# Performance work log

Hardware: AMD Instinct MI355X
Metric: run time of the kernel (lower is better)

## Reference

```python
import jax, jax.numpy as jnp
import numpy as np

BLOCK_SIZE = 32
FP6_E2M3_MAX = 7.5

def _build_fp6_e2m3_grid():
    vals = set()
    for bits in range(64):
        s = (bits >> 5) & 1
        e = (bits >> 3) & 3
        m = bits & 7
        v = (m / 8.0) if e == 0 else (1.0 + m / 8.0) * 2.0 ** (e - 1)
        vals.add(-v if s else v)
    return np.array(sorted(vals), dtype=np.float32)

_GRID = jnp.asarray(_build_fp6_e2m3_grid())  # sorted 1-D fp32 grid (46 unique values)

def _nearest_on_grid(x, grid):
    # round-to-nearest on a sorted grid via searchsorted (matches torch reference)
    idx = jnp.clip(jnp.searchsorted(grid, x), 0, grid.shape[0] - 1)
    idx_lo = jnp.maximum(idx - 1, 0)
    v_hi = grid[idx]
    v_lo = grid[idx_lo]
    return jnp.where(jnp.abs(x - v_lo) <= jnp.abs(x - v_hi), v_lo, v_hi)

def _mx_quantize(t, eps=1e-30):
    # t: (rows, K) fp32, K divisible by BLOCK_SIZE
    rows, K = t.shape
    blocks = t.reshape(rows, K // BLOCK_SIZE, BLOCK_SIZE)
    scales = jnp.maximum(jnp.max(jnp.abs(blocks), axis=-1) / FP6_E2M3_MAX, eps)  # (rows, nb)
    q = _nearest_on_grid(blocks / scales[..., None], _GRID)  # fp6-simulated fp32
    return q, scales

def setup_inputs() -> dict:
    key = jax.random.key(0)
    k1, k2, k3 = jax.random.split(key, 3)
    x = jax.random.normal(k1, (8, 8192, 1024), dtype=jnp.float32)
    weight = jax.random.normal(k2, (1024, 1024), dtype=jnp.float32) * 0.02
    bias = jax.random.normal(k3, (1024,), dtype=jnp.float32) * 0.02
    return {"x": x, "weight": weight, "bias": bias}

def reference(x, weight, bias):
    batch_shape = x.shape[:-1]
    in_features = x.shape[-1]
    x2 = x.astype(jnp.float32).reshape(-1, in_features)      # (N, K)
    w2 = weight.astype(jnp.float32)                           # (J, K)
    xq, xs = _mx_quantize(x2)                                 # (N, nb, bs), (N, nb)
    wq, ws = _mx_quantize(w2)                                 # (J, nb, bs), (J, nb)
    # out[n, j] = sum_b xs[n,b] * ws[j,b] * dot(xq[n,b,:], wq[j,b,:])
    # == dequant(x) @ dequant(w).T  (fold fp32 scales into quantized blocks)
    xd = (xq * xs[..., None]).reshape(x2.shape)
    wd = (wq * ws[..., None]).reshape(w2.shape)
    out = xd @ wd.T + bias
    return out.reshape(*batch_shape, -1)
```

## Files before the change

kernel.cpp:

```cpp
#include <hip/hip_runtime.h>
#include <stdint.h>

#define K_DIM 1024
#define N_DIM 1024
#define M_DIM 65536

typedef __bf16 bf16_t;
typedef __bf16 bf16x8 __attribute__((ext_vector_type(8)));
typedef float f32x4 __attribute__((ext_vector_type(4)));

#define GLOAD_LDS16(g, l) __builtin_amdgcn_global_load_lds( \
    (const __attribute__((address_space(1))) void*)(g),     \
    (__attribute__((address_space(3))) void*)(l), 16, 0, 0)

#define VMCNT(n) asm volatile("s_waitcnt vmcnt(%0)" ::"n"(n) : "memory")
#define LGKM(n) asm volatile("s_waitcnt lgkmcnt(%0)" ::"n"(n) : "memory")
#define SCHEDB() __builtin_amdgcn_sched_barrier(0)

__global__ __launch_bounds__(256) void quant_dequant_kernel(
    const float* __restrict__ in, bf16_t* __restrict__ out, long long nvec) {
  long long i = (long long)blockIdx.x * blockDim.x + threadIdx.x;
  long long stride = (long long)gridDim.x * blockDim.x;
  for (; i < nvec; i += stride) {
    long long base = i * 8;
    f32x4 v0 = *reinterpret_cast<const f32x4*>(in + base);
    f32x4 v1 = *reinterpret_cast<const f32x4*>(in + base + 4);
    float mx = 0.0f;
#pragma unroll
    for (int j = 0; j < 4; ++j) {
      mx = fmaxf(mx, fabsf(v0[j]));
      mx = fmaxf(mx, fabsf(v1[j]));
    }
    mx = fmaxf(mx, __shfl_xor(mx, 1));
    mx = fmaxf(mx, __shfl_xor(mx, 2));
    float s = fmaxf(mx / 7.5f, 1e-30f);
    bf16x8 o;
#pragma unroll
    for (int j = 0; j < 8; ++j) {
      float xv = (j < 4) ? v0[j] : v1[j - 4];
      float y = xv / s;
      float m = fabsf(y);
      float h, hinv;
      if (m < 2.0f)      { h = 0.125f; hinv = 8.0f; }
      else if (m < 4.0f) { h = 0.25f;  hinv = 4.0f; }
      else               { h = 0.5f;   hinv = 2.0f; }
      float n = m * hinv;
      float kf = floorf(n);
      float fr = n - kf;
      float up = (fr > 0.5f || (fr == 0.5f && y < 0.0f)) ? 1.0f : 0.0f;
      float q = fminf((kf + up) * h, 7.5f);
      o[j] = (bf16_t)(copysignf(q, y) * s);
    }
    *reinterpret_cast<bf16x8*>(out + base) = o;
  }
}

__global__ __launch_bounds__(512, 2) void mx_gemm(
    const bf16_t* __restrict__ A, const bf16_t* __restrict__ B,
    const float* __restrict__ bias, float* __restrict__ C) {
  __shared__ char lds[131072];

  const int tid = threadIdx.x;
  const int lane = tid & 63;
  const int wid = tid >> 6;
  const int wm = wid >> 2;
  const int wn = wid & 3;

  const int b = blockIdx.x;
  const int xcd = b & 7;
  const int t = b >> 3;
  const int m_tile = xcd * 32 + (t >> 2);
  const int n_tile = t & 3;

  const int R0 = tid >> 2;
  const int c0 = ((tid & 3) ^ ((tid >> 3) & 3)) * 8;
  const bf16_t* aS0 = A + (size_t)(m_tile * 256 + R0) * K_DIM + c0;
  const bf16_t* aS1 = aS0 + (size_t)128 * K_DIM;
  const bf16_t* bS0 = B + (size_t)(n_tile * 256 + R0) * K_DIM + c0;
  const bf16_t* bS1 = bS0 + (size_t)128 * K_DIM;
  const int dstOff = tid * 16;

#define STAGE(u)                                         \
  {                                                      \
    char* sb_ = lds + ((u) & 3) * 32768;                 \
    const int ko_ = (u) * 32;                            \
    GLOAD_LDS16(aS0 + ko_, sb_ + dstOff);                \
    GLOAD_LDS16(aS1 + ko_, sb_ + 8192 + dstOff);         \
    GLOAD_LDS16(bS0 + ko_, sb_ + 16384 + dstOff);        \
    GLOAD_LDS16(bS1 + ko_, sb_ + 24576 + dstOff);        \
  }

  const int ps = (((lane >> 4) ^ ((lane >> 1) & 3)) << 4);
  const int rowb = (lane & 15) * 64 + ps;
  const int aOff = wm * 8192 + rowb;
  const int bOff = 16384 + wn * 4096 + rowb;

  f32x4 acc[8][4];
#pragma unroll
  for (int i = 0; i < 8; ++i)
#pragma unroll
    for (int j = 0; j < 4; ++j) acc[i][j] = (f32x4)(0.0f);

  bf16x8 bfA[4], bfB[4], afA[4], afB[4], af1[4];

#define PH_A(T, BF, AF0, DO_STG)                                          \
  {                                                                       \
    const char* sb_ = lds + ((T) & 3) * 32768;                            \
    _Pragma("unroll") for (int i = 0; i < 4; ++i) af1[i] =                \
        *reinterpret_cast<const bf16x8*>(sb_ + aOff + 4096 + i * 1024);   \
    if (DO_STG) STAGE((T) + 3);                                           \
    LGKM(4);                                                              \
    SCHEDB();                                                             \
    __builtin_amdgcn_s_setprio(1);                                        \
    _Pragma("unroll") for (int i = 0; i < 4; ++i)                         \
        _Pragma("unroll") for (int j = 0; j < 4; ++j) acc[i][j] =         \
            __builtin_amdgcn_mfma_f32_16x16x32_bf16(AF0[i], BF[j],        \
                                                    acc[i][j], 0, 0, 0);  \
    __builtin_amdgcn_s_setprio(0);                                        \
  }

#define PH_B(T, BF, NBF, NAF0, VMN, DO_PRE)                                  \
  {                                                                          \
    VMCNT(VMN);                                                              \
    LGKM(0);                                                                 \
    __builtin_amdgcn_s_barrier();                                            \
    SCHEDB();                                                                \
    if (DO_PRE) {                                                            \
      const char* sn_ = lds + (((T) + 1) & 3) * 32768;                       \
      _Pragma("unroll") for (int j = 0; j < 4; ++j) NBF[j] =                 \
          *reinterpret_cast<const bf16x8*>(sn_ + bOff + j * 1024);           \
      _Pragma("unroll") for (int i = 0; i < 4; ++i) NAF0[i] =                \
          *reinterpret_cast<const bf16x8*>(sn_ + aOff + i * 1024);           \
    }                                                                        \
    __builtin_amdgcn_s_setprio(1);                                           \
    _Pragma("unroll") for (int i = 0; i < 4; ++i)                            \
        _Pragma("unroll") for (int j = 0; j < 4; ++j) acc[4 + i][j] =        \
            __builtin_amdgcn_mfma_f32_16x16x32_bf16(af1[i], BF[j],           \
                                                    acc[4 + i][j], 0, 0, 0); \
    __builtin_amdgcn_s_setprio(0);                                           \
  }

  STAGE(0);
  STAGE(1);
  STAGE(2);
  VMCNT(8);
  __builtin_amdgcn_s_barrier();
  SCHEDB();
#pragma unroll
  for (int j = 0; j < 4; ++j)
    bfA[j] = *reinterpret_cast<const bf16x8*>(lds + bOff + j * 1024);
#pragma unroll
  for (int i = 0; i < 4; ++i)
    afA[i] = *reinterpret_cast<const bf16x8*>(lds + aOff + i * 1024);

  for (int p = 0; p < 14; ++p) {
    const int u = 2 * p;
    PH_A(u, bfA, afA, true);
    PH_B(u, bfA, bfB, afB, 8, true);
    PH_A(u + 1, bfB, afB, true);
    PH_B(u + 1, bfB, bfA, afA, 8, true);
  }
  PH_A(28, bfA, afA, true);
  PH_B(28, bfA, bfB, afB, 8, true);
  PH_A(29, bfB, afB, false);
  PH_B(29, bfB, bfA, afA, 4, true);
  PH_A(30, bfA, afA, false);
  PH_B(30, bfA, bfB, afB, 0, true);
  PH_A(31, bfB, afB, false);
  LGKM(0);
  SCHEDB();
#pragma unroll
  for (int i = 0; i < 4; ++i)
#pragma unroll
    for (int j = 0; j < 4; ++j)
      acc[4 + i][j] = __builtin_amdgcn_mfma_f32_16x16x32_bf16(
          af1[i], bfB[j], acc[4 + i][j], 0, 0, 0);

  const int col0 = n_tile * 256 + wn * 64 + (lane & 15);
  const int row0 = m_tile * 256 + wm * 128 + ((lane >> 4) << 2);
#pragma unroll
  for (int j = 0; j < 4; ++j) {
    float bv = bias[col0 + j * 16];
#pragma unroll
    for (int m = 0; m < 8; ++m) {
#pragma unroll
      for (int r = 0; r < 4; ++r) {
        C[(size_t)(row0 + m * 16 + r) * N_DIM + col0 + j * 16] =
            acc[m][j][r] + bv;
      }
    }
  }
#undef STAGE
#undef PH_A
#undef PH_B
}

extern "C" void kernel_launch(void* const* d_in, const int* in_sizes, int n_in,
                              void* d_out, int out_size, void* d_ws,
                              size_t ws_size, hipStream_t stream) {
  const float* x = (const float*)d_in[0];
  const float* w = (const float*)d_in[1];
  const float* bias = (const float*)d_in[2];
  float* out = (float*)d_out;

  bf16_t* xd = (bf16_t*)d_ws;
  bf16_t* wd = xd + (size_t)M_DIM * K_DIM;

  quant_dequant_kernel<<<4096, 256, 0, stream>>>(x, xd,
                                                 (long long)M_DIM * K_DIM / 8);
  quant_dequant_kernel<<<512, 256, 0, stream>>>(w, wd,
                                                (long long)K_DIM * N_DIM / 8);

  mx_gemm<<<(M_DIM / 256) * (N_DIM / 256), 512, 0, stream>>>(xd, wd, bias,
                                                             out);
}
```

Baseline: 269.8 us.

## Merge quant launches and restructure GEMM pipeline into split A/B staged phases

The two quant-dequant launches become one kernel whose first 512 blocks handle the weight and the rest handle the activation, saving a launch. The GEMM main loop drops register double-buffering of fragments and now loads B and A fragments from LDS at the start of each phase. Global-to-LDS staging is split into A-half and B-half issues, and extra barriers sit around each MFMA phase. This lowers register pressure and simplifies the loop, but adds barriers and exposes LDS read latency before each MFMA group.

New measurement: 275.2 us. About the same (+2.0%).

```diff
diff --git a/kernel.cpp b/kernel.cpp
--- a/kernel.cpp
+++ b/kernel.cpp
@@ -18,10 +18,21 @@
 #define SCHEDB() __builtin_amdgcn_sched_barrier(0)
 
 __global__ __launch_bounds__(256) void quant_dequant_kernel(
-    const float* __restrict__ in, bf16_t* __restrict__ out, long long nvec) {
-  long long i = (long long)blockIdx.x * blockDim.x + threadIdx.x;
-  long long stride = (long long)gridDim.x * blockDim.x;
-  for (; i < nvec; i += stride) {
+    const float* __restrict__ x, bf16_t* __restrict__ xd, long long nx,
+    const float* __restrict__ w, bf16_t* __restrict__ wd, long long nw) {
+  const float* in;
+  bf16_t* out;
+  long long i, stride, n;
+  if (blockIdx.x < 512) {
+    in = w; out = wd; n = nw;
+    i = (long long)blockIdx.x * blockDim.x + threadIdx.x;
+    stride = 512ll * blockDim.x;
+  } else {
+    in = x; out = xd; n = nx;
+    i = (long long)(blockIdx.x - 512) * blockDim.x + threadIdx.x;
+    stride = (long long)(gridDim.x - 512) * blockDim.x;
+  }
+  for (; i < n; i += stride) {
     long long base = i * 8;
     f32x4 v0 = *reinterpret_cast<const f32x4*>(in + base);
     f32x4 v1 = *reinterpret_cast<const f32x4*>(in + base + 4);
@@ -44,9 +55,9 @@
       if (m < 2.0f)      { h = 0.125f; hinv = 8.0f; }
       else if (m < 4.0f) { h = 0.25f;  hinv = 4.0f; }
       else               { h = 0.5f;   hinv = 2.0f; }
-      float n = m * hinv;
-      float kf = floorf(n);
-      float fr = n - kf;
+      float nn = m * hinv;
+      float kf = floorf(nn);
+      float fr = nn - kf;
       float up = (fr > 0.5f || (fr == 0.5f && y < 0.0f)) ? 1.0f : 0.0f;
       float q = fminf((kf + up) * h, 7.5f);
       o[j] = (bf16_t)(copysignf(q, y) * s);
@@ -80,14 +91,19 @@
   const bf16_t* bS1 = bS0 + (size_t)128 * K_DIM;
   const int dstOff = tid * 16;
 
-#define STAGE(u)                                         \
-  {                                                      \
-    char* sb_ = lds + ((u) & 3) * 32768;                 \
-    const int ko_ = (u) * 32;                            \
-    GLOAD_LDS16(aS0 + ko_, sb_ + dstOff);                \
-    GLOAD_LDS16(aS1 + ko_, sb_ + 8192 + dstOff);         \
-    GLOAD_LDS16(bS0 + ko_, sb_ + 16384 + dstOff);        \
-    GLOAD_LDS16(bS1 + ko_, sb_ + 24576 + dstOff);        \
+#define STAGE_A(u)                                  \
+  {                                                 \
+    char* sd_ = lds + ((u) & 3) * 32768;            \
+    const int ko_ = (u) * 32;                       \
+    GLOAD_LDS16(aS0 + ko_, sd_ + dstOff);           \
+    GLOAD_LDS16(aS1 + ko_, sd_ + 8192 + dstOff);    \
+  }
+#define STAGE_B(u)                                  \
+  {                                                 \
+    char* sd_ = lds + ((u) & 3) * 32768;            \
+    const int ko_ = (u) * 32;                       \
+    GLOAD_LDS16(bS0 + ko_, sd_ + 16384 + dstOff);   \
+    GLOAD_LDS16(bS1 + ko_, sd_ + 24576 + dstOff);   \
   }
 
   const int ps = (((lane >> 4) ^ ((lane >> 1) & 3)) << 4);
@@ -101,80 +117,85 @@
 #pragma unroll
     for (int j = 0; j < 4; ++j) acc[i][j] = (f32x4)(0.0f);
 
-  bf16x8 bfA[4], bfB[4], afA[4], afB[4], af1[4];
-
-#define PH_A(T, BF, AF0, DO_STG)                                          \
+  bf16x8 bf[4], afA[4], afB[4];
+
+#define PH_A(T, VMN, DO_STG)                                              \
   {                                                                       \
     const char* sb_ = lds + ((T) & 3) * 32768;                            \
-    _Pragma("unroll") for (int i = 0; i < 4; ++i) af1[i] =                \
-        *reinterpret_cast<const bf16x8*>(sb_ + aOff + 4096 + i * 1024);   \
-    if (DO_STG) STAGE((T) + 3);                                           \
-    LGKM(4);                                                              \
+    _Pragma("unroll") for (int j = 0; j < 4; ++j) bf[j] =                 \
+        *reinterpret_cast<const bf16x8*>(sb_ + bOff + j * 1024);          \
+    _Pragma("unroll") for (int i = 0; i < 4; ++i) afA[i] =                \
+        *reinterpret_cast<const bf16x8*>(sb_ + aOff + i * 1024);          \
+    if (DO_STG) STAGE_A((T) + 3);                                         \
+    VMCNT(VMN);                                                           \
+    __builtin_amdgcn_s_barrier();                                         \
+    LGKM(0);                                                              \
     SCHEDB();                                                             \
     __builtin_amdgcn_s_setprio(1);                                        \
     _Pragma("unroll") for (int i = 0; i < 4; ++i)                         \
         _Pragma("unroll") for (int j = 0; j < 4; ++j) acc[i][j] =         \
-            __builtin_amdgcn_mfma_f32_16x16x32_bf16(AF0[i], BF[j],        \
+            __builtin_amdgcn_mfma_f32_16x16x32_bf16(afA[i], bf[j],        \
                                                     acc[i][j], 0, 0, 0);  \
     __builtin_amdgcn_s_setprio(0);                                        \
-  }
-
-#define PH_B(T, BF, NBF, NAF0, VMN, DO_PRE)                                  \
+    __builtin_amdgcn_s_barrier();                                         \
+  }
+
+#define PH_B(T, VMN, DO_STG)                                                 \
   {                                                                          \
+    const char* sb_ = lds + ((T) & 3) * 32768;                               \
+    _Pragma("unroll") for (int i = 0; i < 4; ++i) afB[i] =                   \
+        *reinterpret_cast<const bf16x8*>(sb_ + aOff + 4096 + i * 1024);      \
+    if (DO_STG) STAGE_B((T) + 3);                                            \
     VMCNT(VMN);                                                              \
+    __builtin_amdgcn_s_barrier();                                            \
     LGKM(0);                                                                 \
-    __builtin_amdgcn_s_barrier();                                            \
     SCHEDB();                                                                \
-    if (DO_PRE) {                                                            \
-      const char* sn_ = lds + (((T) + 1) & 3) * 32768;                       \
-      _Pragma("unroll") for (int j = 0; j < 4; ++j) NBF[j] =                 \
-          *reinterpret_cast<const bf16x8*>(sn_ + bOff + j * 1024);           \
-      _Pragma("unroll") for (int i = 0; i < 4; ++i) NAF0[i] =                \
-          *reinterpret_cast<const bf16x8*>(sn_ + aOff + i * 1024);           \
-    }                                                                        \
     __builtin_amdgcn_s_setprio(1);                                           \
     _Pragma("unroll") for (int i = 0; i < 4; ++i)                            \
         _Pragma("unroll") for (int j = 0; j < 4; ++j) acc[4 + i][j] =        \
-            __builtin_amdgcn_mfma_f32_16x16x32_bf16(af1[i], BF[j],           \
+            __builtin_amdgcn_mfma_f32_16x16x32_bf16(afB[i], bf[j],           \
                                                     acc[4 + i][j], 0, 0, 0); \
     __builtin_amdgcn_s_setprio(0);                                           \
-  }
-
-  STAGE(0);
-  STAGE(1);
-  STAGE(2);
+    __builtin_amdgcn_s_barrier();                                            \
+  }
+
+  STAGE_A(0); STAGE_B(0);
+  STAGE_A(1); STAGE_B(1);
+  STAGE_A(2); STAGE_B(2);
   VMCNT(8);
   __builtin_amdgcn_s_barrier();
-  SCHEDB();
-#pragma unroll
-  for (int j = 0; j < 4; ++j)
-    bfA[j] = *reinterpret_cast<const bf16x8*>(lds + bOff + j * 1024);
-#pragma unroll
-  for (int i = 0; i < 4; ++i)
-    afA[i] = *reinterpret_cast<const bf16x8*>(lds + aOff + i * 1024);
-
-  for (int p = 0; p < 14; ++p) {
-    const int u = 2 * p;
-    PH_A(u, bfA, afA, true);
-    PH_B(u, bfA, bfB, afB, 8, true);
-    PH_A(u + 1, bfB, afB, true);
-    PH_B(u + 1, bfB, bfA, afA, 8, true);
-  }
-  PH_A(28, bfA, afA, true);
-  PH_B(28, bfA, bfB, afB, 8, true);
-  PH_A(29, bfB, afB, false);
-  PH_B(29, bfB, bfA, afA, 4, true);
-  PH_A(30, bfA, afA, false);
-  PH_B(30, bfA, bfB, afB, 0, true);
-  PH_A(31, bfB, afB, false);
-  LGKM(0);
-  SCHEDB();
-#pragma unroll
-  for (int i = 0; i < 4; ++i)
+
+  for (int kt = 0; kt < 29; ++kt) {
+    PH_A(kt, 8, true);
+    PH_B(kt, 8, true);
+  }
+  PH_A(29, 8, false);
+  PH_B(29, 4, false);
+  PH_A(30, 4, false);
+  PH_B(30, 0, false);
+  {
+    const char* sb_ = lds + (31 & 3) * 32768;
 #pragma unroll
     for (int j = 0; j < 4; ++j)
-      acc[4 + i][j] = __builtin_amdgcn_mfma_f32_16x16x32_bf16(
-          af1[i], bfB[j], acc[4 + i][j], 0, 0, 0);
+      bf[j] = *reinterpret_cast<const bf16x8*>(sb_ + bOff + j * 1024);
+#pragma unroll
+    for (int i = 0; i < 4; ++i)
+      afA[i] = *reinterpret_cast<const bf16x8*>(sb_ + aOff + i * 1024);
+#pragma unroll
+    for (int i = 0; i < 4; ++i)
+      afB[i] = *reinterpret_cast<const bf16x8*>(sb_ + aOff + 4096 + i * 1024);
+    LGKM(0);
+    SCHEDB();
+#pragma unroll
+    for (int i = 0; i < 4; ++i)
+#pragma unroll
+      for (int j = 0; j < 4; ++j) {
+        acc[i][j] = __builtin_amdgcn_mfma_f32_16x16x32_bf16(afA[i], bf[j],
+                                                            acc[i][j], 0, 0, 0);
+        acc[4 + i][j] = __builtin_amdgcn_mfma_f32_16x16x32_bf16(
+            afB[i], bf[j], acc[4 + i][j], 0, 0, 0);
+      }
+  }
 
   const int col0 = n_tile * 256 + wn * 64 + (lane & 15);
   const int row0 = m_tile * 256 + wm * 128 + ((lane >> 4) << 2);
@@ -190,7 +211,8 @@
       }
     }
   }
-#undef STAGE
+#undef STAGE_A
+#undef STAGE_B
 #undef PH_A
 #undef PH_B
 }
@@ -206,10 +228,9 @@
   bf16_t* xd = (bf16_t*)d_ws;
   bf16_t* wd = xd + (size_t)M_DIM * K_DIM;
 
-  quant_dequant_kernel<<<4096, 256, 0, stream>>>(x, xd,
-                                                 (long long)M_DIM * K_DIM / 8);
-  quant_dequant_kernel<<<512, 256, 0, stream>>>(w, wd,
-                                                (long long)K_DIM * N_DIM / 8);
+  quant_dequant_kernel<<<4608, 256, 0, stream>>>(
+      x, xd, (long long)M_DIM * K_DIM / 8, w, wd,
+      (long long)K_DIM * N_DIM / 8);
 
   mx_gemm<<<(M_DIM / 256) * (N_DIM / 256), 512, 0, stream>>>(xd, wd, bias,
                                                              out);
```
